# Performance work log

Hardware: AMD Instinct MI355X
Metric: run time of the kernel (lower is better)

Reference implementation:

```python
import jax, jax.numpy as jnp
import numpy as np

N_NODES = 100000
N_EDGES = 1600000
IN_CH = 1024
FEAT_CH = 128
OUT_CH = 3


def setup_inputs() -> dict:
    key = jax.random.key(0)
    ks = jax.random.split(key, 9)
    features = jax.random.normal(ks[0], (N_NODES, IN_CH), dtype=jnp.float32)
    edges = jax.random.randint(ks[1], (2, N_EDGES), 0, N_NODES, dtype=jnp.int64)
    edges2 = jax.random.randint(ks[2], (2, N_EDGES), 0, N_NODES, dtype=jnp.int64)
    edge_features = jax.random.normal(ks[3], (N_EDGES, 1), dtype=jnp.float32)
    additional_feature = jax.random.normal(ks[4], (N_NODES, 20), dtype=jnp.float32)
    # GCNConv linear weights (glorot-ish scale) and biases
    W1 = jax.random.normal(ks[5], (IN_CH, FEAT_CH), dtype=jnp.float32) * (1.0 / np.sqrt(IN_CH))
    b1 = jnp.zeros((FEAT_CH,), dtype=jnp.float32)
    W2 = jax.random.normal(ks[6], (FEAT_CH, OUT_CH), dtype=jnp.float32) * (1.0 / np.sqrt(FEAT_CH))
    b2 = jnp.zeros((OUT_CH,), dtype=jnp.float32)
    return {"features": features, "edges": edges, "edges2": edges2,
            "edge_features": edge_features, "additional_feature": additional_feature,
            "W1": W1, "b1": b1, "W2": W2, "b2": b2}


def gcn_conv(x, edge_index, W, b, num_nodes):
    """PyG GCNConv: x' = D^{-1/2}(A+I)D^{-1/2} x W + b (self-loops added)."""
    x = x @ W  # project first (cheaper feature dim for aggregation)
    loop = jnp.arange(num_nodes, dtype=edge_index.dtype)
    src = jnp.concatenate([edge_index[0], loop])
    dst = jnp.concatenate([edge_index[1], loop])
    deg = jax.ops.segment_sum(jnp.ones_like(dst, dtype=x.dtype), dst,
                              num_segments=num_nodes)  # >=1 due to self-loops
    dinv = jax.lax.rsqrt(deg)
    norm = dinv[src] * dinv[dst]  # [E+N]
    out = jax.ops.segment_sum(x[src] * norm[:, None], dst, num_segments=num_nodes)
    return out + b


def reference(features, edges, edges2, edge_features, additional_feature, W1, b1, W2, b2):
    # use_additional_channels=False -> features unchanged; edge_features forced to None
    n = features.shape[0]
    x = gcn_conv(features, edges2, W1, b1, n)
    x = jax.nn.relu(x)
    # dropout inactive in eval mode
    return gcn_conv(x, edges2, W2, b2, n)
```

## Files before the change

kernel.cpp:

```cpp
#include <hip/hip_runtime.h>
#include <hip/hip_bf16.h>

typedef __attribute__((ext_vector_type(8))) _Float16 half8;
typedef __attribute__((ext_vector_type(4))) float f32x4;

#define N_NODES 100000
#define N_EDGES 1600000
#define IN_CH 1024
#define FEAT 128
#define CAP 64
#define NDIG 196
#define CAPC 10240
#define NTILES ((N_NODES + 127) / 128)

__global__ void k_prep(const float* __restrict__ W1, _Float16* __restrict__ W1t,
                       int* __restrict__ cursorC) {
    int idx = blockIdx.x * 256 + threadIdx.x;
    if (idx < IN_CH * FEAT) {
        int col = idx & (FEAT - 1);
        int k = idx >> 7;
        W1t[(size_t)col * IN_CH + k] = (_Float16)W1[idx];
    }
    if (idx < NDIG) cursorC[idx] = idx * CAPC;
}

__global__ __launch_bounds__(256) void k_bin(const int4* __restrict__ src4,
                                             const int4* __restrict__ dst4,
                                             int* __restrict__ cursorC,
                                             uint2* __restrict__ recs, int e4) {
    __shared__ int hist[NDIG], segoff[NDIG], lcur[NDIG];
    const int t = threadIdx.x, b = blockIdx.x;
    if (t < NDIG) hist[t] = 0;
    __syncthreads();

    const int base4 = b * 2048;
    int4 sv[8], dv[8];
#pragma unroll
    for (int j = 0; j < 8; ++j) {
        int idx = base4 + j * 256 + t;
        if (idx < e4) { sv[j] = src4[idx]; dv[j] = dst4[idx]; }
        else { sv[j] = (int4){-1,-1,-1,-1}; dv[j] = (int4){-1,-1,-1,-1}; }
    }
#pragma unroll
    for (int j = 0; j < 8; ++j) {
        int dd[4] = {dv[j].x, dv[j].y, dv[j].z, dv[j].w};
        int ss[4] = {sv[j].x, sv[j].y, sv[j].z, sv[j].w};
#pragma unroll
        for (int c = 0; c < 4; ++c)
            if ((unsigned)dd[c] < N_NODES && (unsigned)ss[c] < N_NODES)
                atomicAdd(&hist[dd[c] >> 9], 1);
    }
    __syncthreads();
    if (t < NDIG) {
        segoff[t] = atomicAdd(&cursorC[t], hist[t]);
        lcur[t] = 0;
    }
    __syncthreads();
#pragma unroll
    for (int j = 0; j < 8; ++j) {
        int dd[4] = {dv[j].x, dv[j].y, dv[j].z, dv[j].w};
        int ss[4] = {sv[j].x, sv[j].y, sv[j].z, sv[j].w};
#pragma unroll
        for (int c = 0; c < 4; ++c) {
            if ((unsigned)dd[c] < N_NODES && (unsigned)ss[c] < N_NODES) {
                int dg = dd[c] >> 9;
                int r = atomicAdd(&lcur[dg], 1);
                int pos = segoff[dg] + r;
                if (pos < (dg + 1) * CAPC)
                    recs[pos] = (uint2){(unsigned)ss[c], (unsigned)dd[c]};
            }
        }
    }
}

__global__ __launch_bounds__(256) void k_csr(const int* __restrict__ cursorC,
                                             const uint2* __restrict__ recs,
                                             int* __restrict__ csr,
                                             int* __restrict__ cnt) {
    __shared__ int cl[512];
    const int t = threadIdx.x, d = blockIdx.x;
    for (int j = t; j < 512; j += 256) cl[j] = 0;
    __syncthreads();
    const int base = d * CAPC;
    int n = cursorC[d] - base;
    if (n > CAPC) n = CAPC;
    for (int k = t; k < n; k += 256) {
        uint2 r = recs[base + k];
        int local = (int)r.y & 511;
        int slot = atomicAdd(&cl[local], 1);
        if (slot < CAP) csr[((int)r.y << 6) + slot] = (int)r.x;
    }
    __syncthreads();
    const int node0 = d << 9;
    for (int j = t; j < 512; j += 256) {
        int node = node0 + j;
        if (node < N_NODES) cnt[node] = cl[j] < CAP ? cl[j] : CAP;
    }
}

__global__ __launch_bounds__(256, 4) void k_gemm(const float* __restrict__ A,
                                                 const _Float16* __restrict__ Bt,
                                                 _Float16* __restrict__ H, int M) {
    __shared__ _Float16 Bs[2][128][72];
    const int t = threadIdx.x;
    const int wid = t >> 6, lane = t & 63;
    const int brow0 = blockIdx.x * 128;
    const int NKT = IN_CH / 64;

    f32x4 acc[2][8];
#pragma unroll
    for (int m = 0; m < 2; ++m)
#pragma unroll
        for (int nn = 0; nn < 8; ++nn) acc[m][nn] = (f32x4){0.f, 0.f, 0.f, 0.f};

    int r0 = brow0 + wid * 32 + (lane & 15);
    int r1 = r0 + 16;
    if (r0 >= M) r0 = M - 1;
    if (r1 >= M) r1 = M - 1;
    const int kbase = (lane >> 4) * 8;
    const float* pa0 = A + (size_t)r0 * IN_CH + kbase;
    const float* pa1 = A + (size_t)r1 * IN_CH + kbase;
    const int bcol = t >> 1;
    const int bko = (t & 1) * 32;
    const _Float16* pb = Bt + (size_t)bcol * IN_CH + bko;

    float4 ar[2][2][2];
    half8 af[2][2];
    half8 bst[4];

#define LOAD_A(kt)                                                              \
    {                                                                           \
        _Pragma("unroll") for (int m = 0; m < 2; ++m) {                         \
            const float* p_ = (m ? pa1 : pa0) + (kt) * 64;                      \
            _Pragma("unroll") for (int kk = 0; kk < 2; ++kk) {                  \
                ar[m][kk][0] = *(const float4*)(p_ + kk * 32);                  \
                ar[m][kk][1] = *(const float4*)(p_ + kk * 32 + 4);              \
            }                                                                   \
        }                                                                       \
    }
#define CVT_A()                                                                 \
    {                                                                           \
        _Pragma("unroll") for (int m = 0; m < 2; ++m)                           \
        _Pragma("unroll") for (int kk = 0; kk < 2; ++kk) {                      \
            half8 h;                                                            \
            h[0] = (_Float16)ar[m][kk][0].x; h[1] = (_Float16)ar[m][kk][0].y;   \
            h[2] = (_Float16)ar[m][kk][0].z; h[3] = (_Float16)ar[m][kk][0].w;   \
            h[4] = (_Float16)ar[m][kk][1].x; h[5] = (_Float16)ar[m][kk][1].y;   \
            h[6] = (_Float16)ar[m][kk][1].z; h[7] = (_Float16)ar[m][kk][1].w;   \
            af[m][kk] = h;                                                      \
        }                                                                       \
    }
#define LOAD_B(kt)                                                              \
    {                                                                           \
        const half8* s_ = (const half8*)(pb + (kt) * 64);                       \
        _Pragma("unroll") for (int j = 0; j < 4; ++j) bst[j] = s_[j];           \
    }
#define WRITE_B(buf)                                                            \
    {                                                                           \
        _Pragma("unroll") for (int j = 0; j < 4; ++j)                           \
            *(half8*)(&Bs[buf][bcol][bko + j * 8]) = bst[j];                    \
    }

    LOAD_A(0); LOAD_B(0);
    CVT_A();
    WRITE_B(0);
    __syncthreads();

    for (int kt = 0; kt < NKT; ++kt) {
        const int cur = kt & 1;
        const bool more = (kt + 1 < NKT);
        if (more) { LOAD_B(kt + 1); LOAD_A(kt + 1); }
#pragma unroll
        for (int kk = 0; kk < 2; ++kk) {
            half8 a0 = af[0][kk], a1 = af[1][kk];
#pragma unroll
            for (int nn = 0; nn < 8; ++nn) {
                half8 bb = *(const half8*)(&Bs[cur][nn * 16 + (lane & 15)][kk * 32 + kbase]);
                acc[0][nn] = __builtin_amdgcn_mfma_f32_16x16x32_f16(a0, bb, acc[0][nn], 0, 0, 0);
                acc[1][nn] = __builtin_amdgcn_mfma_f32_16x16x32_f16(a1, bb, acc[1][nn], 0, 0, 0);
            }
        }
        if (more) {
            CVT_A();
            WRITE_B(cur ^ 1);
            __syncthreads();
        }
    }
#undef LOAD_A
#undef CVT_A
#undef LOAD_B
#undef WRITE_B

    int colb = lane & 15, rgrp = (lane >> 4) * 4;
#pragma unroll
    for (int m = 0; m < 2; ++m) {
#pragma unroll
        for (int r = 0; r < 4; ++r) {
            int grow = brow0 + wid * 32 + m * 16 + rgrp + r;
            if (grow < M) {
                _Float16* hp = H + (size_t)grow * FEAT + colb;
#pragma unroll
                for (int nn = 0; nn < 8; ++nn) hp[nn * 16] = (_Float16)acc[m][nn][r];
            }
        }
    }
}

__device__ __forceinline__ float dinv_of(const int* cnt, int i, int& m) {
    m = cnt[i];
    return rsqrtf((float)(m + 1));
}

__global__ __launch_bounds__(256) void k_agg1(const _Float16* __restrict__ H,
                                              const int* __restrict__ csr,
                                              const int* __restrict__ cnt,
                                              const float* __restrict__ b1,
                                              const float* __restrict__ W2,
                                              float* __restrict__ Y, int n) {
    int wid = threadIdx.x >> 6, lane = threadIdx.x & 63;
    int i = blockIdx.x * 4 + wid;
    if (i >= n) return;
    const int g = lane >> 4, u = lane & 15;
    int m;
    float di = dinv_of(cnt, i, m);
    int base = i << 6;

    int sl; float dl;
    if (lane < m) {
        sl = csr[base + lane];
        int cs = cnt[sl];
        dl = rsqrtf((float)(cs + 1));
    } else {
        sl = i;
        dl = (lane == m) ? di : 0.f;
    }
    int mm = (m < 63 ? m : 63) + 1;

    float ax[8];
#pragma unroll
    for (int j = 0; j < 8; ++j) ax[j] = 0.f;

    for (int e = 0; e < mm; e += 8) {
        int i0 = e + g, i1 = e + 4 + g;
        bool v0 = i0 < mm, v1 = i1 < mm;
        int c0i = v0 ? i0 : 0, c1i = v1 ? i1 : 0;
        int s0 = __shfl(sl, c0i);
        float w0 = __shfl(dl, c0i);
        int s1 = __shfl(sl, c1i);
        float w1 = __shfl(dl, c1i);
        if (!v0) { s0 = i; w0 = 0.f; }
        if (!v1) { s1 = i; w1 = 0.f; }
        half8 h0 = *(const half8*)(H + ((size_t)s0 << 7) + u * 8);
        half8 h1 = *(const half8*)(H + ((size_t)s1 << 7) + u * 8);
#pragma unroll
        for (int j = 0; j < 8; ++j) ax[j] += w0 * (float)h0[j] + w1 * (float)h1[j];
    }

#pragma unroll
    for (int j = 0; j < 8; ++j) {
        ax[j] += __shfl_xor(ax[j], 16);
        ax[j] += __shfl_xor(ax[j], 32);
    }

    int c0 = u * 8;
    float y0 = 0.f, y1 = 0.f, y2 = 0.f;
#pragma unroll
    for (int j = 0; j < 8; ++j) {
        float x = di * ax[j] + b1[c0 + j];
        x = x > 0.f ? x : 0.f;
        y0 += x * W2[(c0 + j) * 3 + 0];
        y1 += x * W2[(c0 + j) * 3 + 1];
        y2 += x * W2[(c0 + j) * 3 + 2];
    }
#pragma unroll
    for (int d = 1; d < 16; d <<= 1) {
        y0 += __shfl_xor(y0, d);
        y1 += __shfl_xor(y1, d);
        y2 += __shfl_xor(y2, d);
    }
    if (lane == 0) {
        float* yp = Y + (size_t)i * 4;
        yp[0] = di * y0; yp[1] = di * y1; yp[2] = di * y2;
    }
}

__global__ void k_agg2(const float* __restrict__ Y, const int* __restrict__ csr,
                       const int* __restrict__ cnt, const float* __restrict__ b2,
                       float* __restrict__ out, int n) {
    int i = blockIdx.x * 256 + threadIdx.x;
    if (i >= n) return;
    int m;
    float di = dinv_of(cnt, i, m);
    int base = i << 6;
    const float4* Y4 = (const float4*)Y;
    float4 self = Y4[i];
    float a0 = self.x, a1 = self.y, a2 = self.z;
    int e = 0;
    for (; e + 1 < m; e += 2) {
        int s0 = csr[base + e], s1 = csr[base + e + 1];
        float4 v0 = Y4[s0], v1 = Y4[s1];
        a0 += v0.x + v1.x;
        a1 += v0.y + v1.y;
        a2 += v0.z + v1.z;
    }
    if (e < m) {
        float4 v0 = Y4[csr[base + e]];
        a0 += v0.x; a1 += v0.y; a2 += v0.z;
    }
    out[(size_t)i * 3 + 0] = di * a0 + b2[0];
    out[(size_t)i * 3 + 1] = di * a1 + b2[1];
    out[(size_t)i * 3 + 2] = di * a2 + b2[2];
}

extern "C" void kernel_launch(void* const* d_in, const int* in_sizes, int n_in,
                              void* d_out, int out_size, void* d_ws, size_t ws_size,
                              hipStream_t stream) {
    const float* features = (const float*)d_in[0];
    const int* edges2 = (const int*)d_in[2];
    const float* W1 = (const float*)d_in[5];
    const float* b1 = (const float*)d_in[6];
    const float* W2 = (const float*)d_in[7];
    const float* b2 = (const float*)d_in[8];
    float* out = (float*)d_out;

    const int N = N_NODES, E = N_EDGES;
    const int* srcp = edges2;
    const int* dstp = edges2 + E;

    char* p = (char*)d_ws;
    auto carve = [&](size_t bytes) { char* q = p; p += (bytes + 255) & ~(size_t)255; return q; };
    int* cnt      = (int*)carve(4 * (size_t)N);
    int* cursorC  = (int*)carve(4 * NDIG);
    uint2* recs   = (uint2*)carve(8 * (size_t)NDIG * CAPC);
    int* csr      = (int*)carve(4 * (size_t)N * CAP);
    _Float16* W1t = (_Float16*)carve(2 * (size_t)IN_CH * FEAT);
    _Float16* H   = (_Float16*)carve(2 * (size_t)N * FEAT);
    float* Y      = (float*)carve(16 * (size_t)N);

    k_prep<<<dim3(512), dim3(256), 0, stream>>>(W1, W1t, cursorC);
    k_bin<<<dim3(NDIG), dim3(256), 0, stream>>>(
        (const int4*)srcp, (const int4*)dstp, cursorC, recs, E / 4);
    k_csr<<<dim3(NDIG), dim3(256), 0, stream>>>(cursorC, recs, csr, cnt);
    k_gemm<<<dim3(NTILES), dim3(256), 0, stream>>>(features, W1t, H, N);
    k_agg1<<<dim3((N + 3) / 4), dim3(256), 0, stream>>>(H, csr, cnt, b1, W2, Y, N);
    k_agg2<<<dim3((N + 255) / 256), dim3(256), 0, stream>>>(Y, csr, cnt, b2, out, N);
}
```

Measured before the change: 282.5 us.

## Fuse edge binning and CSR build into GEMM launch with grid barrier

Merges the edge-binning, CSR-building and dense GEMM kernels into one launch. The first NDIG blocks do binning, wait on a global atomic counter until every binning block has finished, then build the CSR. The remaining blocks run the GEMM concurrently in a shared-memory union. This is meant to remove launch gaps and let the latency-bound graph preprocessing overlap the bandwidth-bound GEMM. The risks are a spin-wait deadlock if all 196 binning blocks are not co-resident, and the launch_bounds change from 4 to 2 blocks per CU, which may alter GEMM occupancy and register allocation.

```diff
diff --git a/kernel.cpp b/kernel.cpp
--- a/kernel.cpp
+++ b/kernel.cpp
@@ -14,7 +14,7 @@
 #define NTILES ((N_NODES + 127) / 128)
 
 __global__ void k_prep(const float* __restrict__ W1, _Float16* __restrict__ W1t,
-                       int* __restrict__ cursorC) {
+                       int* __restrict__ cursorC, int* __restrict__ done) {
     int idx = blockIdx.x * 256 + threadIdx.x;
     if (idx < IN_CH * FEAT) {
         int col = idx & (FEAT - 1);
@@ -22,89 +22,97 @@
         W1t[(size_t)col * IN_CH + k] = (_Float16)W1[idx];
     }
     if (idx < NDIG) cursorC[idx] = idx * CAPC;
-}
-
-__global__ __launch_bounds__(256) void k_bin(const int4* __restrict__ src4,
-                                             const int4* __restrict__ dst4,
-                                             int* __restrict__ cursorC,
-                                             uint2* __restrict__ recs, int e4) {
-    __shared__ int hist[NDIG], segoff[NDIG], lcur[NDIG];
-    const int t = threadIdx.x, b = blockIdx.x;
-    if (t < NDIG) hist[t] = 0;
-    __syncthreads();
-
-    const int base4 = b * 2048;
-    int4 sv[8], dv[8];
-#pragma unroll
-    for (int j = 0; j < 8; ++j) {
-        int idx = base4 + j * 256 + t;
-        if (idx < e4) { sv[j] = src4[idx]; dv[j] = dst4[idx]; }
-        else { sv[j] = (int4){-1,-1,-1,-1}; dv[j] = (int4){-1,-1,-1,-1}; }
-    }
-#pragma unroll
-    for (int j = 0; j < 8; ++j) {
-        int dd[4] = {dv[j].x, dv[j].y, dv[j].z, dv[j].w};
-        int ss[4] = {sv[j].x, sv[j].y, sv[j].z, sv[j].w};
-#pragma unroll
-        for (int c = 0; c < 4; ++c)
-            if ((unsigned)dd[c] < N_NODES && (unsigned)ss[c] < N_NODES)
-                atomicAdd(&hist[dd[c] >> 9], 1);
-    }
-    __syncthreads();
-    if (t < NDIG) {
-        segoff[t] = atomicAdd(&cursorC[t], hist[t]);
-        lcur[t] = 0;
-    }
-    __syncthreads();
-#pragma unroll
-    for (int j = 0; j < 8; ++j) {
-        int dd[4] = {dv[j].x, dv[j].y, dv[j].z, dv[j].w};
-        int ss[4] = {sv[j].x, sv[j].y, sv[j].z, sv[j].w};
-#pragma unroll
-        for (int c = 0; c < 4; ++c) {
-            if ((unsigned)dd[c] < N_NODES && (unsigned)ss[c] < N_NODES) {
-                int dg = dd[c] >> 9;
-                int r = atomicAdd(&lcur[dg], 1);
-                int pos = segoff[dg] + r;
-                if (pos < (dg + 1) * CAPC)
-                    recs[pos] = (uint2){(unsigned)ss[c], (unsigned)dd[c]};
+    if (idx == 0) *done = 0;
+}
+
+__global__ __launch_bounds__(256, 2) void k_build_gemm(
+    const float* __restrict__ A, const _Float16* __restrict__ Bt,
+    const int4* __restrict__ src4, const int4* __restrict__ dst4,
+    int* __restrict__ cursorC, uint2* __restrict__ recs,
+    int* __restrict__ csr, int* __restrict__ cnt, int* __restrict__ done,
+    _Float16* __restrict__ H, int M, int e4)
+{
+    __shared__ union {
+        _Float16 Bs[2][128][72];
+        struct { int hist[NDIG], segoff[NDIG], lcur[NDIG]; } bin;
+        int cl[512];
+    } sm;
+    const int t = threadIdx.x;
+
+    if (blockIdx.x < NDIG) {
+        const int b = blockIdx.x;
+        if (t < NDIG) sm.bin.hist[t] = 0;
+        __syncthreads();
+
+        const int base4 = b * 2048;
+        int4 sv[8], dv[8];
+#pragma unroll
+        for (int j = 0; j < 8; ++j) {
+            int idx = base4 + j * 256 + t;
+            if (idx < e4) { sv[j] = src4[idx]; dv[j] = dst4[idx]; }
+            else { sv[j] = (int4){-1,-1,-1,-1}; dv[j] = (int4){-1,-1,-1,-1}; }
+        }
+#pragma unroll
+        for (int j = 0; j < 8; ++j) {
+            int dd[4] = {dv[j].x, dv[j].y, dv[j].z, dv[j].w};
+            int ss[4] = {sv[j].x, sv[j].y, sv[j].z, sv[j].w};
+#pragma unroll
+            for (int c = 0; c < 4; ++c)
+                if ((unsigned)dd[c] < N_NODES && (unsigned)ss[c] < N_NODES)
+                    atomicAdd(&sm.bin.hist[dd[c] >> 9], 1);
+        }
+        __syncthreads();
+        if (t < NDIG) {
+            sm.bin.segoff[t] = atomicAdd(&cursorC[t], sm.bin.hist[t]);
+            sm.bin.lcur[t] = 0;
+        }
+        __syncthreads();
+#pragma unroll
+        for (int j = 0; j < 8; ++j) {
+            int dd[4] = {dv[j].x, dv[j].y, dv[j].z, dv[j].w};
+            int ss[4] = {sv[j].x, sv[j].y, sv[j].z, sv[j].w};
+#pragma unroll
+            for (int c = 0; c < 4; ++c) {
+                if ((unsigned)dd[c] < N_NODES && (unsigned)ss[c] < N_NODES) {
+                    int dg = dd[c] >> 9;
+                    int r = atomicAdd(&sm.bin.lcur[dg], 1);
+                    int pos = sm.bin.segoff[dg] + r;
+                    if (pos < (dg + 1) * CAPC)
+                        recs[pos] = (uint2){(unsigned)ss[c], (unsigned)dd[c]};
+                }
             }
         }
-    }
-}
-
-__global__ __launch_bounds__(256) void k_csr(const int* __restrict__ cursorC,
-                                             const uint2* __restrict__ recs,
-                                             int* __restrict__ csr,
-                                             int* __restrict__ cnt) {
-    __shared__ int cl[512];
-    const int t = threadIdx.x, d = blockIdx.x;
-    for (int j = t; j < 512; j += 256) cl[j] = 0;
-    __syncthreads();
-    const int base = d * CAPC;
-    int n = cursorC[d] - base;
-    if (n > CAPC) n = CAPC;
-    for (int k = t; k < n; k += 256) {
-        uint2 r = recs[base + k];
-        int local = (int)r.y & 511;
-        int slot = atomicAdd(&cl[local], 1);
-        if (slot < CAP) csr[((int)r.y << 6) + slot] = (int)r.x;
-    }
-    __syncthreads();
-    const int node0 = d << 9;
-    for (int j = t; j < 512; j += 256) {
-        int node = node0 + j;
-        if (node < N_NODES) cnt[node] = cl[j] < CAP ? cl[j] : CAP;
-    }
-}
-
-__global__ __launch_bounds__(256, 4) void k_gemm(const float* __restrict__ A,
-                                                 const _Float16* __restrict__ Bt,
-                                                 _Float16* __restrict__ H, int M) {
-    __shared__ _Float16 Bs[2][128][72];
-    const int t = threadIdx.x;
+        __syncthreads();
+        if (t == 0) {
+            __threadfence();
+            __hip_atomic_fetch_add(done, 1, __ATOMIC_RELEASE, __HIP_MEMORY_SCOPE_AGENT);
+            while (__hip_atomic_load(done, __ATOMIC_ACQUIRE, __HIP_MEMORY_SCOPE_AGENT) < NDIG)
+                __builtin_amdgcn_s_sleep(8);
+        }
+        __syncthreads();
+        const int d = blockIdx.x;
+        for (int j = t; j < 512; j += 256) sm.cl[j] = 0;
+        __syncthreads();
+        const int base = d * CAPC;
+        int n = cursorC[d] - base;
+        if (n > CAPC) n = CAPC;
+        for (int k = t; k < n; k += 256) {
+            uint2 r = recs[base + k];
+            int local = (int)r.y & 511;
+            int slot = atomicAdd(&sm.cl[local], 1);
+            if (slot < CAP) csr[((int)r.y << 6) + slot] = (int)r.x;
+        }
+        __syncthreads();
+        const int node0 = d << 9;
+        for (int j = t; j < 512; j += 256) {
+            int node = node0 + j;
+            if (node < N_NODES) cnt[node] = sm.cl[j] < CAP ? sm.cl[j] : CAP;
+        }
+        return;
+    }
+
     const int wid = t >> 6, lane = t & 63;
-    const int brow0 = blockIdx.x * 128;
+    const int brow0 = (blockIdx.x - NDIG) * 128;
     const int NKT = IN_CH / 64;
 
     f32x4 acc[2][8];
@@ -158,7 +166,7 @@
 #define WRITE_B(buf)                                                            \
     {                                                                           \
         _Pragma("unroll") for (int j = 0; j < 4; ++j)                           \
-            *(half8*)(&Bs[buf][bcol][bko + j * 8]) = bst[j];                    \
+            *(half8*)(&sm.Bs[buf][bcol][bko + j * 8]) = bst[j];                 \
     }
 
     LOAD_A(0); LOAD_B(0);
@@ -175,7 +183,7 @@
             half8 a0 = af[0][kk], a1 = af[1][kk];
 #pragma unroll
             for (int nn = 0; nn < 8; ++nn) {
-                half8 bb = *(const half8*)(&Bs[cur][nn * 16 + (lane & 15)][kk * 32 + kbase]);
+                half8 bb = *(const half8*)(&sm.Bs[cur][nn * 16 + (lane & 15)][kk * 32 + kbase]);
                 acc[0][nn] = __builtin_amdgcn_mfma_f32_16x16x32_f16(a0, bb, acc[0][nn], 0, 0, 0);
                 acc[1][nn] = __builtin_amdgcn_mfma_f32_16x16x32_f16(a1, bb, acc[1][nn], 0, 0, 0);
             }
@@ -331,17 +339,17 @@
     auto carve = [&](size_t bytes) { char* q = p; p += (bytes + 255) & ~(size_t)255; return q; };
     int* cnt      = (int*)carve(4 * (size_t)N);
     int* cursorC  = (int*)carve(4 * NDIG);
+    int* done     = (int*)carve(4);
     uint2* recs   = (uint2*)carve(8 * (size_t)NDIG * CAPC);
     int* csr      = (int*)carve(4 * (size_t)N * CAP);
     _Float16* W1t = (_Float16*)carve(2 * (size_t)IN_CH * FEAT);
     _Float16* H   = (_Float16*)carve(2 * (size_t)N * FEAT);
     float* Y      = (float*)carve(16 * (size_t)N);
 
-    k_prep<<<dim3(512), dim3(256), 0, stream>>>(W1, W1t, cursorC);
-    k_bin<<<dim3(NDIG), dim3(256), 0, stream>>>(
-        (const int4*)srcp, (const int4*)dstp, cursorC, recs, E / 4);
-    k_csr<<<dim3(NDIG), dim3(256), 0, stream>>>(cursorC, recs, csr, cnt);
-    k_gemm<<<dim3(NTILES), dim3(256), 0, stream>>>(features, W1t, H, N);
+    k_prep<<<dim3(512), dim3(256), 0, stream>>>(W1, W1t, cursorC, done);
+    k_build_gemm<<<dim3(NDIG + NTILES), dim3(256), 0, stream>>>(
+        features, W1t, (const int4*)srcp, (const int4*)dstp,
+        cursorC, recs, csr, cnt, done, H, N, E / 4);
     k_agg1<<<dim3((N + 3) / 4), dim3(256), 0, stream>>>(H, csr, cnt, b1, W2, Y, N);
     k_agg2<<<dim3((N + 255) / 256), dim3(256), 0, stream>>>(Y, csr, cnt, b2, out, N);
 }
```

Measured after the change: 269.5 us. -4.6%, faster.
